# Performance work log

Hardware: AMD Instinct MI355X
Metric: run time of the kernel (lower is better)

## Reference

```python
import jax, jax.numpy as jnp
import numpy as np

B, T, N, D, FF, E, L, K = 4, 12, 2000, 16, 64, 4, 2, 2
EA, H = 3000, 3
BETA, CW = 0.01, 0.001


def setup_inputs() -> dict:
    key = jax.random.key(0)
    ks = iter(jax.random.split(key, 40))
    nrm = lambda shape, s=0.02: jax.random.normal(next(ks), shape, jnp.float32) * s
    inp = {}
    inp['x'] = jax.random.normal(next(ks), (B, T, N), jnp.float32)
    inp['velo'] = jax.random.uniform(next(ks), (B, T, N), jnp.float32)
    inp['adj_haversine'] = jax.random.uniform(next(ks), (N, N), jnp.float32) + 0.05
    inp['laplacian_diff'] = jax.random.normal(next(ks), (N, N), jnp.float32)
    inp['laplacian_heat'] = jax.random.normal(next(ks), (N, N), jnp.float32)
    inp['start_w'] = nrm((1, D)); inp['start_b'] = jnp.zeros((D,), jnp.float32)
    inp['gate_w'] = nrm((L, D, E))
    inp['exp_w1'] = nrm((L, E, D, FF)); inp['exp_b1'] = jnp.zeros((L, E, FF), jnp.float32)
    inp['exp_w2'] = nrm((L, E, FF, D)); inp['exp_b2'] = jnp.zeros((L, E, D), jnp.float32)
    inp['proj_w'] = nrm((T * D, T)); inp['proj_b'] = jnp.zeros((T,), jnp.float32)
    inp['lt_w'] = nrm((N, EA)); inp['lt_b'] = jnp.zeros((EA,), jnp.float32)
    inp['qkv_w'] = nrm((EA, 3 * EA)); inp['qkv_b'] = jnp.zeros((3 * EA,), jnp.float32)
    inp['attn_out_w'] = nrm((EA, EA)); inp['attn_out_b'] = jnp.zeros((EA,), jnp.float32)
    inp['ll_w'] = nrm((EA, N)); inp['ll_b'] = jnp.zeros((N,), jnp.float32)
    inp['p2_w'] = nrm((T, T)); inp['p2_b'] = jnp.zeros((T,), jnp.float32)
    return inp


def reference(x, velo, adj_haversine, laplacian_diff, laplacian_heat, start_w, start_b,
              gate_w, exp_w1, exp_b1, exp_w2, exp_b2, proj_w, proj_b, lt_w, lt_b,
              qkv_w, qkv_b, attn_out_w, attn_out_b, ll_w, ll_b, p2_w, p2_b):
    # start_fc: [B,T,N,1] -> [B,T,N,D]
    out = x[..., None] @ start_w + start_b
    balance = jnp.float32(0.0)
    cv = lambda v: v.var() / (v.mean() ** 2 + 1e-10)
    for l in range(L):  # AMS mixture-of-experts stack (noisy top-k gating, eval mode)
        feat = out.mean(axis=(1, 2))                      # [B,D]
        logits = feat @ gate_w[l]                          # [B,E]
        topv, topi = jax.lax.top_k(logits, K)
        g = jax.nn.softmax(topv, axis=-1)
        gates = jnp.zeros((B, E), out.dtype).at[jnp.arange(B)[:, None], topi].set(g)
        h = jax.nn.gelu(jnp.einsum('btnd,edf->ebtnf', out, exp_w1[l]) + exp_b1[l][:, None, None, None, :])
        y = jnp.einsum('ebtnf,efd->ebtnd', h, exp_w2[l]) + exp_b2[l][:, None, None, None, :]
        out = out + jnp.einsum('be,ebtnd->btnd', gates, y)  # residual_connection
        imp = gates.sum(0)
        load = (gates > 0).astype(out.dtype).sum(0)
        balance = balance + cv(imp) + cv(load)
    # wavelet layer: 1-level smoothing split along time
    low = lambda z: 0.5 * (z + jnp.roll(z, 1, axis=1))
    low_T = low(x)
    high_V = velo - low(velo)
    # navier-stokes-style graph laplacian from velocities
    v0 = velo[0, 0]                                        # [N]
    G = jnp.maximum(0.0, v0[:, None] / adj_haversine)
    G = jnp.where(jnp.isinf(G), 0.0, G)
    lap_ns = jnp.diag(G.sum(1)) - G
    std = lambda m: (m - m.mean()) / m.std()
    lap_d = std(laplacian_diff); lap_h = std(laplacian_heat)
    lap_ns = jnp.nan_to_num(std(lap_ns))
    # trunk projection: [B,T,N,D] -> [B,T,N]
    outp = (out.transpose(0, 2, 1, 3).reshape(B, N, T * D) @ proj_w + proj_b).transpose(0, 2, 1)
    # laplacian-fused matmuls
    r1 = low_T @ lap_d; r2 = high_V @ lap_ns; r3 = low_T @ lap_h
    rng01 = lambda m: (m - m.min()) / jnp.maximum(m.max() - m.min(), 1e-8)
    lin = lambda m: (rng01(m) @ lt_w + lt_b).transpose(1, 0, 2)   # [T,B,EA]
    r1, r2, r3 = lin(r1), lin(r2), lin(r3)
    hd = EA // H
    wq, wk, wv = jnp.split(qkv_w, 3, axis=1)
    bq, bk, bv = jnp.split(qkv_b, 3)
    def mha(q, k, v):
        qh = (q @ wq + bq).reshape(T, B, H, hd)
        kh = (k @ wk + bk).reshape(T, B, H, hd)
        vh = (v @ wv + bv).reshape(T, B, H, hd)
        sc = jnp.einsum('sbhd,tbhd->bhst', qh, kh) * (1.0 / np.sqrt(hd))
        a = jax.nn.softmax(sc, axis=-1)
        o = jnp.einsum('bhst,tbhd->sbhd', a, vh).reshape(T, B, EA)
        return o @ attn_out_w + attn_out_b
    o1 = mha(r1, r2, r3); o2 = mha(r2, r3, r1); o3 = mha(r3, r1, r2)
    back = lambda o: (o @ ll_w + ll_b).transpose(1, 0, 2)         # [B,T,N]
    out2 = BETA * (back(o1) + back(o2) + back(o3))
    out2 = (out2.reshape(-1, T) @ p2_w + p2_b).reshape(B, N, T).transpose(0, 2, 1)
    out_3 = outp + out2
    # contrastive loss between trunk and laplacian branch
    f1 = outp.transpose(0, 2, 1).reshape(B * N, T)
    f2 = out2.transpose(0, 2, 1).reshape(B * N, T)
    nz = lambda f: f / jnp.maximum(jnp.linalg.norm(f, axis=1, keepdims=True), 1e-12)
    sim = (nz(f1) @ nz(f2).T) / 0.1                               # [8000, 8000]
    closs = -jnp.mean(jnp.diagonal(jax.nn.log_softmax(sim, axis=1)))
    return out_3, balance, CW * closs
```

## Files before the change

### kernel.cpp

```cpp
#include <hip/hip_runtime.h>
#include <math.h>

namespace {
constexpr int B_ = 4, T_ = 12, N_ = 2000, D_ = 16, FF_ = 64, E_ = 4, L_ = 2;
constexpr int EA_ = 3000, H_ = 3, HD_ = EA_ / H_;
constexpr int BT_ = B_ * T_;
constexpr int R3_ = 3 * BT_;
constexpr long long NN_ = (long long)N_ * N_;
constexpr int BTN_ = B_ * T_ * N_;
constexpr float BETA_ = 0.01f, CW_ = 0.001f;
constexpr int RKS_ = 20;
constexpr int RKC_ = 100;
constexpr int KP3 = 3008;
constexpr int KP2 = 2016;

constexpr int W2_QN = 141, W2_QK = 47;
constexpr int W2_AN = 47,  W2_AK = 47;
constexpr int W2_LN = 32,  W2_LK = 47;
constexpr int W2_WN = 47,  W2_WK = 32;
constexpr int W2_C0 = W2_QN * W2_QK;
constexpr int W2_C1 = W2_C0 + W2_AN * W2_AK;
constexpr int W2_C2 = W2_C1 + W2_LN * W2_LK;
constexpr int W2_TOT = W2_C2 + W2_WN * W2_WK;

constexpr size_t OFF_OUT4 = 0;
constexpr size_t OFF_LOWT = OFF_OUT4 + (size_t)BTN_ * D_;
constexpr size_t OFF_HVT  = OFF_LOWT + BTN_;
constexpr size_t OFF_ALIN = OFF_HVT + BTN_;
constexpr size_t OFF_RT   = OFF_ALIN + (size_t)N_ * R3_;
constexpr size_t OFF_P    = OFF_RT + (size_t)EA_ * R3_;
constexpr size_t OFF_AOT  = OFF_P + (size_t)R3_ * 3 * EA_;
constexpr size_t OFF_OT   = OFF_AOT + (size_t)EA_ * R3_;
constexpr size_t OFF_O2P  = OFF_OT + (size_t)EA_ * R3_;
constexpr size_t OFF_OUTP = OFF_O2P + BTN_;
constexpr size_t OFF_O2F  = OFF_OUTP + BTN_;
constexpr size_t OFF_LI   = OFF_O2F + BTN_;
constexpr size_t OFF_S    = OFF_LI + 8000;
constexpr size_t OFF_RSL  = OFF_S + 2000;
constexpr size_t OFF_RSH  = OFF_RSL + 48;
constexpr size_t OFF_STP  = OFF_RSH + 48;
constexpr size_t OFF_STAT = OFF_STP + 3072;
constexpr size_t OFF_MMP  = OFF_STAT + 8;
constexpr size_t OFF_AB   = OFF_MMP + 384;
constexpr size_t OFF_CSP  = OFF_AB + 8;
constexpr size_t OFF_CS   = OFF_CSP + 48000;
constexpr size_t OFF_FEAT = OFF_CS + 3000;
constexpr size_t OFF_GATE = OFF_FEAT + 64;
constexpr size_t OFF_BAL  = OFF_GATE + 16;
constexpr size_t OFF_PART = ((OFF_BAL + 1 + 255) & ~(size_t)255);
constexpr size_t PARTCAP  = 6000000;
constexpr size_t OFF_BT_Q  = OFF_PART + PARTCAP;
constexpr size_t OFF_BT_A  = OFF_BT_Q + (size_t)9000 * KP3 / 2;
constexpr size_t OFF_BT_L  = OFF_BT_A + (size_t)3000 * KP3 / 2;
constexpr size_t OFF_BT_W  = OFF_BT_L + (size_t)2000 * KP3 / 2;
constexpr size_t OFF_AT_LIN= OFF_BT_W + (size_t)3000 * KP2 / 2;
constexpr size_t OFF_AT_Q  = OFF_AT_LIN + (size_t)R3_ * KP2 / 2;
constexpr size_t OFF_AT_AO = OFF_AT_Q + (size_t)R3_ * KP3 / 2;
constexpr size_t OFF_AT_LL = OFF_AT_AO + (size_t)R3_ * KP3 / 2;
constexpr size_t OFF_G1B   = OFF_AT_LL + (size_t)R3_ * KP3 / 2;
constexpr size_t OFF_G2B   = OFF_G1B + 128000;
}

typedef __attribute__((ext_vector_type(8))) short short8;
typedef __attribute__((ext_vector_type(4))) float f32x4;

__device__ __forceinline__ float waveReduceSum(float v) {
  for (int off = 32; off; off >>= 1) v += __shfl_down(v, off);
  return v;
}

__device__ __forceinline__ unsigned short f2bf(float x) {
  unsigned int u = __float_as_uint(x);
  unsigned int r = (u + 0x7FFFu + ((u >> 16) & 1u)) >> 16;
  return (unsigned short)r;
}

__device__ __forceinline__ void fma16(float* __restrict__ acc,
                                      const float4* __restrict__ a4, float bv) {
#pragma unroll
  for (int r4 = 0; r4 < 4; ++r4) {
    float4 av = a4[r4];
    acc[r4 * 4 + 0] = fmaf(av.x, bv, acc[r4 * 4 + 0]);
    acc[r4 * 4 + 1] = fmaf(av.y, bv, acc[r4 * 4 + 1]);
    acc[r4 * 4 + 2] = fmaf(av.z, bv, acc[r4 * 4 + 2]);
    acc[r4 * 4 + 3] = fmaf(av.w, bv, acc[r4 * 4 + 3]);
  }
}

__global__ void k_init(float* ws) {
  if (threadIdx.x == 0) ws[OFF_BAL] = 0.f;
}

__global__ void k_start(const float* __restrict__ x, const float* __restrict__ sw,
                        const float* __restrict__ sb, float* __restrict__ out4) {
  int i = blockIdx.x * 256 + threadIdx.x;
  if (i >= BTN_ * D_) return;
  int d = i & 15;
  out4[i] = fmaf(x[i >> 4], sw[d], sb[d]);
}

__global__ void k_feat(const float* __restrict__ out4, float* __restrict__ feat) {
  int b = blockIdx.x >> 4, d = blockIdx.x & 15;
  float s = 0.f;
  for (int tn = threadIdx.x; tn < T_ * N_; tn += 256)
    s += out4[((size_t)b * T_ * N_ + tn) * D_ + d];
  __shared__ float red[4];
  s = waveReduceSum(s);
  if ((threadIdx.x & 63) == 0) red[threadIdx.x >> 6] = s;
  __syncthreads();
  if (threadIdx.x == 0)
    feat[blockIdx.x] = (red[0] + red[1] + red[2] + red[3]) * (1.f / (T_ * N_));
}

__global__ void k_gate(const float* __restrict__ feat, const float* __restrict__ gw,
                       float* __restrict__ ws, int l) {
  __shared__ float lg[B_ * E_];
  int tid = threadIdx.x;
  if (tid < B_ * E_) {
    int b = tid >> 2, e = tid & 3;
    float s = 0.f;
    for (int d = 0; d < D_; ++d) s = fmaf(feat[b * D_ + d], gw[(l * D_ + d) * E_ + e], s);
    lg[tid] = s;
  }
  __syncthreads();
  if (tid == 0) {
    float* gates = ws + OFF_GATE;
    float imp[E_] = {0, 0, 0, 0}, load[E_] = {0, 0, 0, 0};
    for (int i = 0; i < B_ * E_; ++i) gates[i] = 0.f;
    for (int b = 0; b < B_; ++b) {
      const float* lb = lg + b * E_;
      int i1 = 0; float v1 = lb[0];
      for (int e = 1; e < E_; ++e) if (lb[e] > v1) { v1 = lb[e]; i1 = e; }
      int i2 = -1; float v2 = -1e30f;
      for (int e = 0; e < E_; ++e) { if (e == i1) continue; if (lb[e] > v2) { v2 = lb[e]; i2 = e; } }
      float e2 = expf(v2 - v1);
      float den = 1.f + e2;
      float g1 = 1.f / den, g2 = e2 / den;
      gates[b * E_ + i1] = g1; gates[b * E_ + i2] = g2;
      imp[i1] += g1; imp[i2] += g2; load[i1] += 1.f; load[i2] += 1.f;
    }
    float bal = 0.f;
    float m = 0.f; for (int e = 0; e < E_; ++e) m += imp[e]; m *= 0.25f;
    float v = 0.f; for (int e = 0; e < E_; ++e) { float d = imp[e] - m; v += d * d; } v *= 0.25f;
    bal += v / (m * m + 1e-10f);
    m = 0.f; for (int e = 0; e < E_; ++e) m += load[e]; m *= 0.25f;
    v = 0.f; for (int e = 0; e < E_; ++e) { float d = load[e] - m; v += d * d; } v *= 0.25f;
    bal += v / (m * m + 1e-10f);
    ws[OFF_BAL] += bal;
  }
}

__global__ void k_expert(float* __restrict__ out4, const float* __restrict__ w1,
                         const float* __restrict__ b1, const float* __restrict__ w2,
                         const float* __restrict__ b2, const float* __restrict__ ws, int l) {
  int b = blockIdx.y;
  int tn = blockIdx.x * 256 + threadIdx.x;
  if (tn >= T_ * N_) return;
  float* row = out4 + ((size_t)b * T_ * N_ + tn) * D_;
  float r[D_], acc[D_];
#pragma unroll
  for (int d = 0; d < D_; ++d) { r[d] = row[d]; acc[d] = r[d]; }
  const float* gates = ws + OFF_GATE;
  for (int e = 0; e < E_; ++e) {
    float g = gates[b * E_ + e];
    if (g <= 0.f) continue;
    const float* W1 = w1 + (size_t)(l * E_ + e) * D_ * FF_;
    const float* B1 = b1 + (size_t)(l * E_ + e) * FF_;
    const float* W2 = w2 + (size_t)(l * E_ + e) * FF_ * D_;
    const float* B2 = b2 + (size_t)(l * E_ + e) * D_;
#pragma unroll 4
    for (int f = 0; f < FF_; ++f) {
      float p = B1[f];
#pragma unroll
      for (int d = 0; d < D_; ++d) p = fmaf(r[d], W1[d * FF_ + f], p);
      float c2 = 1.5957691216057308f * (p + 0.044715f * p * p * p);
      float e1 = __expf(-c2);
      float hv = p * __builtin_amdgcn_rcpf(1.f + e1);
      float gh = g * hv;
#pragma unroll
      for (int d = 0; d < D_; ++d) acc[d] = fmaf(gh, W2[f * D_ + d], acc[d]);
    }
#pragma unroll
    for (int d = 0; d < D_; ++d) acc[d] = fmaf(g, B2[d], acc[d]);
  }
#pragma unroll
  for (int d = 0; d < D_; ++d) row[d] = acc[d];
}

__global__ void k_wavelet(const float* __restrict__ x, const float* __restrict__ velo,
                          float* __restrict__ lowT, float* __restrict__ hvT) {
  int i = blockIdx.x * 256 + threadIdx.x;
  if (i >= BTN_) return;
  int b = i / (T_ * N_);
  int t = (i / N_) % T_;
  int n = i % N_;
  int ip = b * T_ * N_ + ((t + T_ - 1) % T_) * N_ + n;
  int row = t * B_ + b;
  lowT[(size_t)n * BT_ + row] = 0.5f * (x[i] + x[ip]);
  hvT[(size_t)n * BT_ + row] = 0.5f * (velo[i] - velo[ip]);
}

__global__ void k_rowsum(const float* __restrict__ lowT, const float* __restrict__ hvT,
                         float* __restrict__ ws) {
  int which = blockIdx.x / BT_;
  int row = blockIdx.x % BT_;
  const float* M = which ? hvT : lowT;
  float s = 0.f;
  for (int n = threadIdx.x; n < N_; n += 256) s += M[(size_t)n * BT_ + row];
  __shared__ float red[4];
  s = waveReduceSum(s);
  if ((threadIdx.x & 63) == 0) red[threadIdx.x >> 6] = s;
  __syncthreads();
  if (threadIdx.x == 0) ws[(which ? OFF_RSH : OFF_RSL) + row] = red[0] + red[1] + red[2] + red[3];
}

__global__ void k_S(const float* __restrict__ adj, const float* __restrict__ v0,
                    float* __restrict__ S) {
  int m = blockIdx.x;
  float vm = v0[m];
  const float* a = adj + (size_t)m * N_;
  float s = 0.f;
  for (int n = threadIdx.x; n < N_; n += 256) s += vm / a[n];
  __shared__ float red[4];
  s = waveReduceSum(s);
  if ((threadIdx.x & 63) == 0) red[threadIdx.x >> 6] = s;
  __syncthreads();
  if (threadIdx.x == 0) S[m] = red[0] + red[1] + red[2] + red[3];
}

__global__ void k_stats3(const float* __restrict__ lapd, const float* __restrict__ laph,
                         const float* __restrict__ adj, const float* __restrict__ v0,
                         const float* __restrict__ S, float* __restrict__ stp) {
  int z = blockIdx.z;
  float s = 0.f, ss = 0.f;
  if (z < 2) {
    const float* M = z ? laph : lapd;
    for (long long i = blockIdx.x * 256 + threadIdx.x; i < NN_; i += 512 * 256) {
      float v = M[i];
      s += v; ss = fmaf(v, v, ss);
    }
  } else {
    for (long long i = blockIdx.x * 256 + threadIdx.x; i < NN_; i += 512 * 256) {
      int m = (int)(i / N_), n = (int)(i % N_);
      float e = -(v0[m] / adj[i]);
      if (m == n) e += S[m];
      s += e; ss = fmaf(e, e, ss);
    }
  }
  __shared__ float r1[4], r2[4];
  for (int off = 32; off; off >>= 1) { s += __shfl_down(s, off); ss += __shfl_down(ss, off); }
  if ((threadIdx.x & 63) == 0) { r1[threadIdx.x >> 6] = s; r2[threadIdx.x >> 6] = ss; }
  __syncthreads();
  if (threadIdx.x == 0) {
    float* p = stp + (size_t)z * 1024;
    p[blockIdx.x * 2] = r1[0] + r1[1] + r1[2] + r1[3];
    p[blockIdx.x * 2 + 1] = r2[0] + r2[1] + r2[2] + r2[3];
  }
}

__global__ void k_stats2(const float* __restrict__ stp, float* __restrict__ stat) {
  int z = blockIdx.x;
  const float* part = stp + (size_t)z * 1024;
  float s = 0.f, ss = 0.f;
  for (int i = threadIdx.x; i < 512; i += 256) { s += part[i * 2]; ss += part[i * 2 + 1]; }
  __shared__ float r1[4], r2[4];
  for (int off = 32; off; off >>= 1) { s += __shfl_down(s, off); ss += __shfl_down(ss, off); }
  if ((threadIdx.x & 63) == 0) { r1[threadIdx.x >> 6] = s; r2[threadIdx.x >> 6] = ss; }
  __syncthreads();
  if (threadIdx.x == 0) {
    float su = r1[0] + r1[1] + r1[2] + r1[3];
    float sq = r2[0] + r2[1] + r2[2] + r2[3];
    float mu = su * (1.f / (float)NN_);
    float var = sq * (1.f / (float)NN_) - mu * mu;
    stat[2 * z] = mu;
    stat[2 * z + 1] = 1.f / sqrtf(var);
  }
}

__global__ __launch_bounds__(256) void k_rgemm3(
    const float* __restrict__ lowT, const float* __restrict__ hvT,
    const float* __restrict__ lapd, const float* __restrict__ laph,
    const float* __restrict__ adj, const float* __restrict__ v0,
    const float* __restrict__ S, float* __restrict__ part) {
  int zz = blockIdx.z;
  int z = zz / 3, rg = zz % 3;
  int col = blockIdx.x * 256 + threadIdx.x;
  int m0 = blockIdx.y * RKC_;
  int m1 = min(N_, m0 + RKC_);
  float acc[16];
#pragma unroll
  for (int r = 0; r < 16; ++r) acc[r] = 0.f;
  if (col < N_) {
    const float* Abase = (z == 1 ? hvT : lowT);
    const float* ap = Abase + (size_t)m0 * BT_ + rg * 16;
    if (z != 1) {
      const float* Bm = z ? laph : lapd;
      const float* bp = Bm + (size_t)m0 * N_ + col;
      int len = m1 - m0;
      int ng = len >> 3;
      float bc[8];
      if (ng > 0) {
#pragma unroll
        for (int u = 0; u < 8; ++u) bc[u] = bp[(size_t)u * N_];
      }
      for (int gi = 0; gi < ng; ++gi) {
        float bn[8];
        bool more = (gi + 1 < ng);
        if (more) {
#pragma unroll
          for (int u = 0; u < 8; ++u) bn[u] = bp[(size_t)(8 + u) * N_];
        }
#pragma unroll
        for (int u = 0; u < 8; ++u)
          fma16(acc, (const float4*)(ap + (size_t)u * BT_), bc[u]);
        ap += (size_t)8 * BT_;
        bp += (size_t)8 * N_;
        if (more) {
#pragma unroll
          for (int u = 0; u < 8; ++u) bc[u] = bn[u];
        }
      }
      for (int m = m0 + (ng << 3); m < m1; ++m) {
        fma16(acc, (const float4*)ap, *bp);
        ap += BT_;
        bp += N_;
      }
    } else {
      const float* jp = adj + (size_t)m0 * N_ + col;
      int len = m1 - m0;
      int ng = len >> 3;
      float jc[8];
      if (ng > 0) {
#pragma unroll
        for (int u = 0; u < 8; ++u) jc[u] = jp[(size_t)u * N_];
      }
      int m = m0;
      for (int gi = 0; gi < ng; ++gi) {
        float jn[8];
        bool more = (gi + 1 < ng);
        if (more) {
#pragma unroll
          for (int u = 0; u < 8; ++u) jn[u] = jp[(size_t)(8 + u) * N_];
        }
#pragma unroll
        for (int u = 0; u < 8; ++u) {
          float bv = -(v0[m + u] / jc[u]);
          if (m + u == col) bv += S[m + u];
          fma16(acc, (const float4*)(ap + (size_t)u * BT_), bv);
        }
        m += 8;
        ap += (size_t)8 * BT_;
        jp += (size_t)8 * N_;
        if (more) {
#pragma unroll
          for (int u = 0; u < 8; ++u) jc[u] = jn[u];
        }
      }
      for (; m < m1; ++m) {
        float bv = -(v0[m] / (*jp));
        if (m == col) bv += S[m];
        fma16(acc, (const float4*)ap, bv);
        ap += BT_;
        jp += N_;
      }
    }
    float* pp = part + (((size_t)z * RKS_ + blockIdx.y) * BT_ + rg * 16) * N_ + col;
#pragma unroll
    for (int r = 0; r < 16; ++r) pp[(size_t)r * N_] = acc[r];
  }
}

__global__ void k_epiR3(const float* __restrict__ part, float* __restrict__ ws,
                        unsigned short* __restrict__ atl) {
  int z = blockIdx.z;
  int n = blockIdx.x * 256 + threadIdx.x;
  int row = blockIdx.y;
  if (n >= KP2) return;
  int arow = z * BT_ + row;
  if (n >= N_) { atl[(size_t)arow * KP2 + n] = 0; return; }
  const float* base = part + (size_t)z * RKS_ * BT_ * N_;
  float s = 0.f;
  for (int ks = 0; ks < RKS_; ++ks) s += base[((size_t)(ks * BT_ + row)) * N_ + n];
  int statIdx = (z == 0) ? 0 : (z == 1 ? 4 : 2);
  size_t rsOff = (z == 1) ? OFF_RSH : OFF_RSL;
  float mu = ws[OFF_STAT + statIdx], isd = ws[OFF_STAT + statIdx + 1];
  float val = (s - mu * ws[rsOff + row]) * isd;
  ws[OFF_ALIN + (size_t)n * R3_ + arow] = val;
  atl[(size_t)arow * KP2 + n] = f2bf(val);
}

__global__ __launch_bounds__(256) void k_wtrans4(
    const float* __restrict__ W0, const float* __restrict__ W1,
    const float* __restrict__ W2, const float* __restrict__ W3,
    unsigned short* __restrict__ T0, unsigned short* __restrict__ T1,
    unsigned short* __restrict__ T2, unsigned short* __restrict__ T3) {
  int bid = blockIdx.x;
  const float* W; unsigned short* Wt; int K, Nc, Kp, rel, NT;
  if (bid < W2_C0)      { W = W0; Wt = T0; K = EA_; Nc = 3 * EA_; Kp = KP3; rel = bid;         NT = W2_QN; }
  else if (bid < W2_C1) { W = W1; Wt = T1; K = EA_; Nc = EA_;     Kp = KP3; rel = bid - W2_C0; NT = W2_AN; }
  else if (bid < W2_C2) { W = W2; Wt = T2; K = EA_; Nc = N_;      Kp = KP3; rel = bid - W2_C1; NT = W2_LN; }
  else                  { W = W3; Wt = T3; K = N_;  Nc = EA_;     Kp = KP2; rel = bid - W2_C2; NT = W2_WN; }
  int kTile = rel / NT, nTile = rel % NT;
  int k0 = kTile * 64, n0 = nTile * 64;
  __shared__ float t[64][65];
  int nx = threadIdx.x & 15;
  int kk = threadIdx.x >> 4;
  bool fullN = (n0 + 64 <= Nc);
#pragma unroll
  for (int i = 0; i < 4; ++i) {
    int kl = kk + 16 * i;
    int k = k0 + kl;
    int n = n0 + 4 * nx;
    float4 v = {0.f, 0.f, 0.f, 0.f};
    if (k < K) {
      if (fullN) {
        v = *(const float4*)(W + (size_t)k * Nc + n);
      } else {
        if (n + 3 < Nc)      v = *(const float4*)(W + (size_t)k * Nc + n);
        else {
          if (n     < Nc) v.x = W[(size_t)k * Nc + n];
          if (n + 1 < Nc) v.y = W[(size_t)k * Nc + n + 1];
          if (n + 2 < Nc) v.z = W[(size_t)k * Nc + n + 2];
          if (n + 3 < Nc) v.w = W[(size_t)k * Nc + n + 3];
        }
      }
    }
    t[4 * nx + 0][kl] = v.x;
    t[4 * nx + 1][kl] = v.y;
    t[4 * nx + 2][kl] = v.z;
    t[4 * nx + 3][kl] = v.w;
  }
  __syncthreads();
  int kq = threadIdx.x & 15;
  int ny = threadIdx.x >> 4;
  int k = k0 + 4 * kq;
#pragma unroll
  for (int i = 0; i < 4; ++i) {
    int nl = ny + 16 * i;
    int n = n0 + nl;
    if (n < Nc && k + 3 < Kp) {
      unsigned int w0 = ((unsigned int)f2bf(t[nl][4 * kq + 1]) << 16) | f2bf(t[nl][4 * kq + 0]);
      unsigned int w1 = ((unsigned int)f2bf(t[nl][4 * kq + 3]) << 16) | f2bf(t[nl][4 * kq + 2]);
      uint2 u; u.x = w0; u.y = w1;
      *(uint2*)(Wt + (size_t)n * Kp + k) = u;
    }
  }
}

__global__ __launch_bounds__(256, 4) void k_mfma(
    const unsigned short* __restrict__ At, const unsigned short* __restrict__ Bt,
    float* __restrict__ part, int Nc, int Kp, int stepsTot, int stepChunk) {
  int lane = threadIdx.x & 63;
  int w = threadIdx.x >> 6;
  int lr = lane & 15, lo = lane >> 4;
  int gcol = blockIdx.x * 64 + w * 16 + lr;
  int bcol = min(gcol, Nc - 1);
  int s0 = blockIdx.y * stepChunk;
  int s1 = min(stepsTot, s0 + stepChunk);
  f32x4 acc[9];
#pragma unroll
  for (int mt = 0; mt < 9; ++mt) {
    acc[mt][0] = 0.f; acc[mt][1] = 0.f; acc[mt][2] = 0.f; acc[mt][3] = 0.f;
  }
  const unsigned short* bp = Bt + (size_t)bcol * Kp + (size_t)s0 * 32 + lo * 8;
  const unsigned short* ap = At + (size_t)lr * Kp + (size_t)s0 * 32 + lo * 8;
  for (int s = s0; s < s1; ++s) {
    short8 b = *(const short8*)bp;
#pragma unroll
    for (int mt = 0; mt < 9; ++mt) {
      short8 a = *(const short8*)(ap + (size_t)mt * 16 * Kp);
      acc[mt] = __builtin_amdgcn_mfma_f32_16x16x32_bf16(a, b, acc[mt], 0, 0, 0);
    }
    bp += 32;
    ap += 32;
  }
  if (gcol < Nc) {
#pragma unroll
    for (int mt = 0; mt < 9; ++mt) {
      int row = mt * 16 + lo * 4;
      float* pp = part + ((size_t)blockIdx.y * R3_ + row) * Nc + gcol;
      pp[0] = acc[mt][0];
      pp[(size_t)Nc] = acc[mt][1];
      pp[2 * (size_t)Nc] = acc[mt][2];
      pp[3 * (size_t)Nc] = acc[mt][3];
    }
  }
}

__global__ void k_minmax(const float* __restrict__ alin, float* __restrict__ mmp) {
  int g = blockIdx.y;
  float mn = 3.4e38f, mx = -3.4e38f;
  for (int i = blockIdx.x * 256 + threadIdx.x; i < N_ * BT_; i += 64 * 256) {
    int n = i / BT_, r = i % BT_;
    float v = alin[(size_t)n * R3_ + g * BT_ + r];
    mn = fminf(mn, v); mx = fmaxf(mx, v);
  }
  __shared__ float rn[4], rx[4];
  for (int off = 32; off; off >>= 1) {
    mn = fminf(mn, __shfl_down(mn, off));
    mx = fmaxf(mx, __shfl_down(mx, off));
  }
  if ((threadIdx.x & 63) == 0) { rn[threadIdx.x >> 6] = mn; rx[threadIdx.x >> 6] = mx; }
  __syncthreads();
  if (threadIdx.x == 0) {
    mn = fminf(fminf(rn[0], rn[1]), fminf(rn[2], rn[3]));
    mx = fmaxf(fmaxf(rx[0], rx[1]), fmaxf(rx[2], rx[3]));
    mmp[(size_t)(g * 64 + blockIdx.x) * 2] = mn;
    mmp[(size_t)(g * 64 + blockIdx.x) * 2 + 1] = mx;
  }
}

__global__ void k_minmax2(float* __restrict__ ws) {
  int g = blockIdx.x;
  int i = threadIdx.x;
  float mn = ws[OFF_MMP + (size_t)(g * 64 + i) * 2];
  float mx = ws[OFF_MMP + (size_t)(g * 64 + i) * 2 + 1];
  for (int off = 32; off; off >>= 1) {
    mn = fminf(mn, __shfl_down(mn, off));
    mx = fmaxf(mx, __shfl_down(mx, off));
  }
  if (i == 0) {
    float denom = fmaxf(mx - mn, 1e-8f);
    float a = 1.f / denom;
    ws[OFF_AB + g * 2] = a;
    ws[OFF_AB + g * 2 + 1] = -mn * a;
  }
}

__global__ void k_colsum(const float* __restrict__ ltw, float* __restrict__ csp) {
  int e = blockIdx.x * 256 + threadIdx.x;
  int ks = blockIdx.y;
  if (e >= EA_) return;
  float s = 0.f;
  for (int n = ks * 125; n < (ks + 1) * 125; ++n) s += ltw[(size_t)n * EA_ + e];
  csp[(size_t)ks * EA_ + e] = s;
}
__global__ void k_colsum2(float* __restrict__ ws) {
  int e = blockIdx.x * 256 + threadIdx.x;
  if (e >= EA_) return;
  float s = 0.f;
  for (int ks = 0; ks < 16; ++ks) s += ws[OFF_CSP + (size_t)ks * EA_ + e];
  ws[OFF_CS + e] = s;
}

__global__ void k_epiLin(const float* __restrict__ part, const float* __restrict__ ltb,
                         float* __restrict__ ws, unsigned short* __restrict__ atq,
                         int ksplit) {
  int e = blockIdx.x * 256 + threadIdx.x;
  int row = blockIdx.y;
  if (e >= KP3) return;
  if (e >= EA_) { atq[(size_t)row * KP3 + e] = 0; return; }
  float s = 0.f;
  for (int ks = 0; ks < ksplit; ++ks) s += part[((size_t)(ks * R3_ + row)) * EA_ + e];
  int g = row / BT_;
  float a = ws[OFF_AB + g * 2], bb = ws[OFF_AB + g * 2 + 1];
  float val = fmaf(a, s, fmaf(bb, ws[OFF_CS + e], ltb[e]));
  atq[(size_t)row * KP3 + e] = f2bf(val);
}

__global__ void k_epiQkv(const float* __restrict__ part, const float* __restrict__ qkvb,
                         float* __restrict__ P, int ksplit) {
  int c = blockIdx.x * 256 + threadIdx.x;
  int row = blockIdx.y;
  if (c >= 3 * EA_) return;
  float s = 0.f;
  for (int ks = 0; ks < ksplit; ++ks) s += part[((size_t)(ks * R3_ + row)) * (3 * EA_) + c];
  P[(size_t)row * (3 * EA_) + c] = s + qkvb[c];
}

__global__ void k_attn(const float* __restrict__ P, unsigned short* __restrict__ atao) {
  int mha = blockIdx.y;
  int s_ = blockIdx.x / (B_ * H_);
  int rem = blockIdx.x % (B_ * H_);
  int b = rem / H_, h = rem % H_;
  const int pq[3] = {0, 1, 2}, pk[3] = {1, 2, 0}, pv[3] = {2, 0, 1};
  const float* qrow = P + ((size_t)(pq[mha] * BT_ + s_ * B_ + b)) * (3 * EA_) + h * HD_;
  __shared__ float sc[T_];
  int w = threadIdx.x >> 6, lane = threadIdx.x & 63;
  for (int t = w; t < T_; t += 4) {
    const float* krow = P + ((size_t)(pk[mha] * BT_ + t * B_ + b)) * (3 * EA_) + EA_ + h * HD_;
    float p = 0.f;
    for (int d = lane; d < HD_; d += 64) p = fmaf(qrow[d], krow[d], p);
    p = waveReduceSum(p);
    if (lane == 0) sc[t] = p * 0.031622776601683794f;
  }
  __syncthreads();
  float a[T_];
  float m = sc[0];
#pragma unroll
  for (int t = 1; t < T_; ++t) m = fmaxf(m, sc[t]);
  float sum = 0.f;
#pragma unroll
  for (int t = 0; t < T_; ++t) { a[t] = expf(sc[t] - m); sum += a[t]; }
  float inv = 1.f / sum;
#pragma unroll
  for (int t = 0; t < T_; ++t) a[t] *= inv;
  int orow = mha * BT_ + s_ * B_ + b;
  for (int d = threadIdx.x; d < HD_; d += 256) {
    float o = 0.f;
#pragma unroll
    for (int t = 0; t < T_; ++t)
      o = fmaf(a[t], P[((size_t)(pv[mha] * BT_ + t * B_ + b)) * (3 * EA_) + 2 * EA_ + h * HD_ + d], o);
    atao[(size_t)orow * KP3 + h * HD_ + d] = f2bf(o);
  }
  if (h == 0 && threadIdx.x < 8) atao[(size_t)orow * KP3 + EA_ + threadIdx.x] = 0;
}

__global__ void k_epiAO(const float* __restrict__ part, const float* __restrict__ aob,
                        unsigned short* __restrict__ atll, int ksplit) {
  int c = blockIdx.x * 256 + threadIdx.x;
  int row = blockIdx.y;
  if (c >= KP3) return;
  if (c >= EA_) { atll[(size_t)row * KP3 + c] = 0; return; }
  float s = 0.f;
  for (int ks = 0; ks < ksplit; ++ks) s += part[((size_t)(ks * R3_ + row)) * EA_ + c];
  atll[(size_t)row * KP3 + c] = f2bf(s + aob[c]);
}

__global__ void k_epiLL(const float* __restrict__ part, const float* __restrict__ llb,
                        float* __restrict__ o2p, int ksplit) {
  int n = blockIdx.x * 256 + threadIdx.x;
  int row = blockIdx.y;
  if (n >= N_) return;
  float s = 0.f;
  for (int g = 0; g < 3; ++g)
    for (int ks = 0; ks < ksplit; ++ks)
      s += part[((size_t)(ks * R3_ + g * BT_ + row)) * N_ + n];
  int t = row / B_, b = row % B_;
  o2p[(size_t)b * (T_ * N_) + t * N_ + n] = BETA_ * (s + 3.f * llb[n]);
}

__global__ void k_proj(const float* __restrict__ out4, const float* __restrict__ pw,
                       const float* __restrict__ pb, float* __restrict__ outp) {
  int i = blockIdx.x * 256 + threadIdx.x;
  if (i >= BTN_) return;
  int b = i / (T_ * N_);
  int t = (i / N_) % T_;
  int n = i % N_;
  float acc = pb[t];
  for (int t2 = 0; t2 < T_; ++t2) {
    const float* o = out4 + ((size_t)(b * T_ + t2) * N_ + n) * D_;
#pragma unroll
    for (int d = 0; d < D_; ++d) acc = fmaf(o[d], pw[(t2 * D_ + d) * T_ + t], acc);
  }
  outp[i] = acc;
}

__global__ void k_p2(const float* __restrict__ o2p, const float* __restrict__ p2w,
                     const float* __restrict__ p2b, float* __restrict__ o2f) {
  int i = blockIdx.x * 256 + threadIdx.x;
  if (i >= BTN_) return;
  int b = i / (T_ * N_);
  int t = (i / N_) % T_;
  int n = i % N_;
  float acc = p2b[t];
  const float* src = o2p + (size_t)b * (T_ * N_) + (size_t)n * T_;
#pragma unroll
  for (int c = 0; c < T_; ++c) acc = fmaf(src[c], p2w[c * T_ + t], acc);
  o2f[i] = acc;
}

__global__ void k_fng(const float* __restrict__ outp, const float* __restrict__ o2f,
                      float* __restrict__ dout, unsigned short* __restrict__ g1b,
                      unsigned short* __restrict__ g2b) {
  int r = blockIdx.x * 256 + threadIdx.x;
  if (r >= B_ * N_) return;
  int b = r / N_, n = r % N_;
  float v1[T_], v2[T_];
  float s1 = 0.f, s2 = 0.f;
#pragma unroll
  for (int t = 0; t < T_; ++t) {
    size_t idx = (size_t)b * T_ * N_ + (size_t)t * N_ + n;
    v1[t] = outp[idx];
    v2[t] = o2f[idx];
    dout[idx] = v1[t] + v2[t];
    s1 = fmaf(v1[t], v1[t], s1);
    s2 = fmaf(v2[t], v2[t], s2);
  }
  float n1 = fmaxf(sqrtf(s1), 1e-12f), n2 = fmaxf(sqrtf(s2), 1e-12f);
  float i1 = 10.f / n1, i2 = 1.f / n2;
  unsigned short q[32], z[32];
#pragma unroll
  for (int t = 0; t < T_; ++t) { q[t] = f2bf(v1[t] * i1); z[t] = f2bf(v2[t] * i2); }
#pragma unroll
  for (int t = T_; t < 32; ++t) { q[t] = 0; z[t] = 0; }
  short8* qd = (short8*)(g1b + (size_t)r * 32);
  short8* zd = (short8*)(g2b + (size_t)r * 32);
#pragma unroll
  for (int c = 0; c < 4; ++c) {
    short8 pv, pz;
#pragma unroll
    for (int e = 0; e < 8; ++e) { pv[e] = (short)q[c * 8 + e]; pz[e] = (short)z[c * 8 + e]; }
    qd[c] = pv;
    zd[c] = pz;
  }
}

__global__ __launch_bounds__(256) void k_lsemf(const unsigned short* __restrict__ g1b,
                                               const unsigned short* __restrict__ g2b,
                                               float* __restrict__ psm,
                                               float* __restrict__ psd) {
  int lane = threadIdx.x & 63, w = threadIdx.x >> 6;
  int lr = lane & 15, lo = lane >> 4;
  int i0 = blockIdx.x * 16;
  int slice = blockIdx.y * 4 + w;
  short8 a = *(const short8*)(g1b + (size_t)(i0 + lr) * 32 + lo * 8);
  float sm[4] = {0.f, 0.f, 0.f, 0.f};
  float sd[4] = {0.f, 0.f, 0.f, 0.f};
  for (int t = slice; t < 500; t += 16) {
    int j0 = t * 16;
    short8 b = *(const short8*)(g2b + (size_t)(j0 + lr) * 32 + lo * 8);
    f32x4 acc = {0.f, 0.f, 0.f, 0.f};
    acc = __builtin_amdgcn_mfma_f32_16x16x32_bf16(a, b, acc, 0, 0, 0);
#pragma unroll
    for (int rg = 0; rg < 4; ++rg) {
      float s = acc[rg];
      sm[rg] += __expf(s);
      if (j0 + lr == i0 + lo * 4 + rg) sd[rg] = s;
    }
  }
#pragma unroll
  for (int off = 1; off < 16; off <<= 1) {
#pragma unroll
    for (int rg = 0; rg < 4; ++rg) {
      sm[rg] += __shfl_xor(sm[rg], off);
      sd[rg] += __shfl_xor(sd[rg], off);
    }
  }
  __shared__ float lsm[4][16], lsd[4][16];
  if (lr == 0) {
#pragma unroll
    for (int rg = 0; rg < 4; ++rg) {
      lsm[w][lo * 4 + rg] = sm[rg];
      lsd[w][lo * 4 + rg] = sd[rg];
    }
  }
  __syncthreads();
  if (threadIdx.x < 16) {
    float m = lsm[0][threadIdx.x] + lsm[1][threadIdx.x] + lsm[2][threadIdx.x] + lsm[3][threadIdx.x];
    float d = lsd[0][threadIdx.x] + lsd[1][threadIdx.x] + lsd[2][threadIdx.x] + lsd[3][threadIdx.x];
    psm[(size_t)blockIdx.y * 8000 + i0 + threadIdx.x] = m;
    psd[(size_t)blockIdx.y * 8000 + i0 + threadIdx.x] = d;
  }
}

__global__ __launch_bounds__(1024) void k_lsefin(const float* __restrict__ psm,
                                                 const float* __restrict__ psd,
                                                 const float* __restrict__ ws,
                                                 float* __restrict__ dout) {
  float acc = 0.f;
  for (int r = threadIdx.x; r < B_ * N_; r += 1024) {
    float sm = psm[r] + psm[8000 + r] + psm[16000 + r] + psm[24000 + r];
    float sd = psd[r] + psd[8000 + r] + psd[16000 + r] + psd[24000 + r];
    acc += sd - logf(sm);
  }
  __shared__ float red[16];
  acc = waveReduceSum(acc);
  if ((threadIdx.x & 63) == 0) red[threadIdx.x >> 6] = acc;
  __syncthreads();
  if (threadIdx.x == 0) {
    float s = 0.f;
    for (int i = 0; i < 16; ++i) s += red[i];
    float closs = -s * (1.f / (B_ * N_));
    dout[BTN_] = ws[OFF_BAL];
    dout[BTN_ + 1] = CW_ * closs;
  }
}

extern "C" void kernel_launch(void* const* d_in, const int* in_sizes, int n_in,
                              void* d_out, int out_size, void* d_ws, size_t ws_size,
                              hipStream_t stream) {
  const float* x    = (const float*)d_in[0];
  const float* velo = (const float*)d_in[1];
  const float* adj  = (const float*)d_in[2];
  const float* lapd = (const float*)d_in[3];
  const float* laph = (const float*)d_in[4];
  const float* sw   = (const float*)d_in[5];
  const float* sb   = (const float*)d_in[6];
  const float* gw   = (const float*)d_in[7];
  const float* ew1  = (const float*)d_in[8];
  const float* eb1  = (const float*)d_in[9];
  const float* ew2  = (const float*)d_in[10];
  const float* eb2  = (const float*)d_in[11];
  const float* pw   = (const float*)d_in[12];
  const float* pb   = (const float*)d_in[13];
  const float* ltw  = (const float*)d_in[14];
  const float* ltb  = (const float*)d_in[15];
  const float* qkvw = (const float*)d_in[16];
  const float* qkvb = (const float*)d_in[17];
  const float* aow  = (const float*)d_in[18];
  const float* aob  = (const float*)d_in[19];
  const float* llw  = (const float*)d_in[20];
  const float* llb  = (const float*)d_in[21];
  const float* p2w  = (const float*)d_in[22];
  const float* p2b  = (const float*)d_in[23];
  float* ws = (float*)d_ws;
  float* dout = (float*)d_out;
  const float* v0 = velo;
  float* part = ws + OFF_PART;
  unsigned short* btQ  = (unsigned short*)(ws + OFF_BT_Q);
  unsigned short* btA  = (unsigned short*)(ws + OFF_BT_A);
  unsigned short* btL  = (unsigned short*)(ws + OFF_BT_L);
  unsigned short* btW  = (unsigned short*)(ws + OFF_BT_W);
  unsigned short* atLin = (unsigned short*)(ws + OFF_AT_LIN);
  unsigned short* atQ   = (unsigned short*)(ws + OFF_AT_Q);
  unsigned short* atAO  = (unsigned short*)(ws + OFF_AT_AO);
  unsigned short* atLL  = (unsigned short*)(ws + OFF_AT_LL);
  unsigned short* g1b   = (unsigned short*)(ws + OFF_G1B);
  unsigned short* g2b   = (unsigned short*)(ws + OFF_G2B);
  dim3 b256(256);

  k_init<<<dim3(1), dim3(64), 0, stream>>>(ws);

  k_wtrans4<<<dim3(W2_TOT), b256, 0, stream>>>(qkvw, aow, llw, ltw, btQ, btA, btL, btW);

  k_start<<<dim3((BTN_ * D_ + 255) / 256), b256, 0, stream>>>(x, sw, sb, ws + OFF_OUT4);

  for (int l = 0; l < L_; ++l) {
    k_feat<<<dim3(B_ * D_), b256, 0, stream>>>(ws + OFF_OUT4, ws + OFF_FEAT);
    k_gate<<<dim3(1), dim3(64), 0, stream>>>(ws + OFF_FEAT, gw, ws, l);
    k_expert<<<dim3((T_ * N_ + 255) / 256, B_), b256, 0, stream>>>(ws + OFF_OUT4, ew1, eb1, ew2, eb2, ws, l);
  }

  k_wavelet<<<dim3((BTN_ + 255) / 256), b256, 0, stream>>>(x, velo, ws + OFF_LOWT, ws + OFF_HVT);
  k_rowsum<<<dim3(2 * BT_), b256, 0, stream>>>(ws + OFF_LOWT, ws + OFF_HVT, ws);
  k_S<<<dim3(N_), b256, 0, stream>>>(adj, v0, ws + OFF_S);

  k_stats3<<<dim3(512, 1, 3), b256, 0, stream>>>(lapd, laph, adj, v0, ws + OFF_S, ws + OFF_STP);
  k_stats2<<<dim3(3), b256, 0, stream>>>(ws + OFF_STP, ws + OFF_STAT);

  k_rgemm3<<<dim3(8, RKS_, 9), b256, 0, stream>>>(ws + OFF_LOWT, ws + OFF_HVT, lapd, laph,
                                                  adj, v0, ws + OFF_S, part);
  k_epiR3<<<dim3(8, 48, 3), b256, 0, stream>>>(part, ws, atLin);

  k_minmax<<<dim3(64, 3), b256, 0, stream>>>(ws + OFF_ALIN, ws + OFF_MMP);
  k_minmax2<<<dim3(3), dim3(64), 0, stream>>>(ws);
  k_colsum<<<dim3(12, 16), b256, 0, stream>>>(ltw, ws + OFF_CSP);
  k_colsum2<<<dim3(12), b256, 0, stream>>>(ws);

  k_mfma<<<dim3(47, 12), b256, 0, stream>>>(atLin, btW, part, EA_, KP2, KP2 / 32, 6);
  k_epiLin<<<dim3(12, 144), b256, 0, stream>>>(part, ltb, ws, atQ, 12);

  k_mfma<<<dim3(141, 4), b256, 0, stream>>>(atQ, btQ, part, 3 * EA_, KP3, KP3 / 32, 24);
  k_epiQkv<<<dim3(36, 144), b256, 0, stream>>>(part, qkvb, ws + OFF_P, 4);

  k_attn<<<dim3(T_ * B_ * H_, 3), b256, 0, stream>>>(ws + OFF_P, atAO);

  k_mfma<<<dim3(47, 12), b256, 0, stream>>>(atAO, btA, part, EA_, KP3, KP3 / 32, 8);
  k_epiAO<<<dim3(12, 144), b256, 0, stream>>>(part, aob, atLL, 12);

  k_mfma<<<dim3(32, 16), b256, 0, stream>>>(atLL, btL, part, N_, KP3, KP3 / 32, 6);
  k_epiLL<<<dim3(8, 48), b256, 0, stream>>>(part, llb, ws + OFF_O2P, 16);

  k_proj<<<dim3((BTN_ + 255) / 256), b256, 0, stream>>>(ws + OFF_OUT4, pw, pb, ws + OFF_OUTP);
  k_p2<<<dim3((BTN_ + 255) / 256), b256, 0, stream>>>(ws + OFF_O2P, p2w, p2b, ws + OFF_O2F);

  k_fng<<<dim3((B_ * N_ + 255) / 256), b256, 0, stream>>>(ws + OFF_OUTP, ws + OFF_O2F, dout, g1b, g2b);

  k_lsemf<<<dim3(500, 4), b256, 0, stream>>>(g1b, g2b, part, part + 32000);
  k_lsefin<<<dim3(1), dim3(1024), 0, stream>>>(part, part + 32000, ws, dout);
}
```

Before: 586.8 us.

## Fuse fp32-to-bf16 weight transpose into MFMA GEMM via LDS staging

Removes the separate weight transpose/convert kernel and instead has the GEMM kernel load fp32 weights directly, convert them to bf16 and stage them transposed in double-buffered LDS per K-step. This removes writing and re-reading a full bf16 copy of all large weight matrices each call. In exchange, each K-step now needs a block-wide barrier and conversion work inside the GEMM loop.

Result: faster. 555.5 us (-5.3%).

```diff
diff --git a/kernel.cpp b/kernel.cpp
--- a/kernel.cpp
+++ b/kernel.cpp
@@ -13,15 +13,6 @@
 constexpr int RKC_ = 100;
 constexpr int KP3 = 3008;
 constexpr int KP2 = 2016;
-
-constexpr int W2_QN = 141, W2_QK = 47;
-constexpr int W2_AN = 47,  W2_AK = 47;
-constexpr int W2_LN = 32,  W2_LK = 47;
-constexpr int W2_WN = 47,  W2_WK = 32;
-constexpr int W2_C0 = W2_QN * W2_QK;
-constexpr int W2_C1 = W2_C0 + W2_AN * W2_AK;
-constexpr int W2_C2 = W2_C1 + W2_LN * W2_LK;
-constexpr int W2_TOT = W2_C2 + W2_WN * W2_WK;
 
 constexpr size_t OFF_OUT4 = 0;
 constexpr size_t OFF_LOWT = OFF_OUT4 + (size_t)BTN_ * D_;
@@ -49,11 +40,7 @@
 constexpr size_t OFF_BAL  = OFF_GATE + 16;
 constexpr size_t OFF_PART = ((OFF_BAL + 1 + 255) & ~(size_t)255);
 constexpr size_t PARTCAP  = 6000000;
-constexpr size_t OFF_BT_Q  = OFF_PART + PARTCAP;
-constexpr size_t OFF_BT_A  = OFF_BT_Q + (size_t)9000 * KP3 / 2;
-constexpr size_t OFF_BT_L  = OFF_BT_A + (size_t)3000 * KP3 / 2;
-constexpr size_t OFF_BT_W  = OFF_BT_L + (size_t)2000 * KP3 / 2;
-constexpr size_t OFF_AT_LIN= OFF_BT_W + (size_t)3000 * KP2 / 2;
+constexpr size_t OFF_AT_LIN= OFF_PART + PARTCAP;
 constexpr size_t OFF_AT_Q  = OFF_AT_LIN + (size_t)R3_ * KP2 / 2;
 constexpr size_t OFF_AT_AO = OFF_AT_Q + (size_t)R3_ * KP3 / 2;
 constexpr size_t OFF_AT_LL = OFF_AT_AO + (size_t)R3_ * KP3 / 2;
@@ -389,91 +376,75 @@
   atl[(size_t)arow * KP2 + n] = f2bf(val);
 }
 
-__global__ __launch_bounds__(256) void k_wtrans4(
-    const float* __restrict__ W0, const float* __restrict__ W1,
-    const float* __restrict__ W2, const float* __restrict__ W3,
-    unsigned short* __restrict__ T0, unsigned short* __restrict__ T1,
-    unsigned short* __restrict__ T2, unsigned short* __restrict__ T3) {
-  int bid = blockIdx.x;
-  const float* W; unsigned short* Wt; int K, Nc, Kp, rel, NT;
-  if (bid < W2_C0)      { W = W0; Wt = T0; K = EA_; Nc = 3 * EA_; Kp = KP3; rel = bid;         NT = W2_QN; }
-  else if (bid < W2_C1) { W = W1; Wt = T1; K = EA_; Nc = EA_;     Kp = KP3; rel = bid - W2_C0; NT = W2_AN; }
-  else if (bid < W2_C2) { W = W2; Wt = T2; K = EA_; Nc = N_;      Kp = KP3; rel = bid - W2_C1; NT = W2_LN; }
-  else                  { W = W3; Wt = T3; K = N_;  Nc = EA_;     Kp = KP2; rel = bid - W2_C2; NT = W2_WN; }
-  int kTile = rel / NT, nTile = rel % NT;
-  int k0 = kTile * 64, n0 = nTile * 64;
-  __shared__ float t[64][65];
-  int nx = threadIdx.x & 15;
-  int kk = threadIdx.x >> 4;
-  bool fullN = (n0 + 64 <= Nc);
-#pragma unroll
-  for (int i = 0; i < 4; ++i) {
-    int kl = kk + 16 * i;
-    int k = k0 + kl;
-    int n = n0 + 4 * nx;
-    float4 v = {0.f, 0.f, 0.f, 0.f};
-    if (k < K) {
-      if (fullN) {
-        v = *(const float4*)(W + (size_t)k * Nc + n);
-      } else {
-        if (n + 3 < Nc)      v = *(const float4*)(W + (size_t)k * Nc + n);
-        else {
-          if (n     < Nc) v.x = W[(size_t)k * Nc + n];
-          if (n + 1 < Nc) v.y = W[(size_t)k * Nc + n + 1];
-          if (n + 2 < Nc) v.z = W[(size_t)k * Nc + n + 2];
-          if (n + 3 < Nc) v.w = W[(size_t)k * Nc + n + 3];
+__global__ __launch_bounds__(256) void k_mfmaW(
+    const unsigned short* __restrict__ At, const float* __restrict__ W,
+    float* __restrict__ part, int Nc, int Kp, int K, int stepChunk) {
+  __shared__ unsigned int lds[2][64][21];
+  int tid = threadIdx.x;
+  int lane = tid & 63, w = tid >> 6;
+  int lr = lane & 15, lo = lane >> 4;
+  int colBase = blockIdx.x * 64;
+  int gcol = colBase + w * 16 + lr;
+  int stepsTot = Kp / 32;
+  int s0 = blockIdx.y * stepChunk;
+  int s1 = min(stepsTot, s0 + stepChunk);
+  int cg = tid & 15, kr2 = tid >> 4;
+  int c0l = 4 * cg;
+  bool fullC = (colBase + 64 <= Nc);
+
+  f32x4 acc[9];
+#pragma unroll
+  for (int mt = 0; mt < 9; ++mt) {
+    acc[mt][0] = 0.f; acc[mt][1] = 0.f; acc[mt][2] = 0.f; acc[mt][3] = 0.f;
+  }
+
+  auto stage = [&](int s, int buf) {
+    int kA = s * 32 + 2 * kr2;
+    int kB = kA + 1;
+    float4 r0 = {0.f, 0.f, 0.f, 0.f}, r1 = {0.f, 0.f, 0.f, 0.f};
+    int c0 = colBase + c0l;
+    if (fullC) {
+      if (kA < K) r0 = *(const float4*)(W + (size_t)kA * Nc + c0);
+      if (kB < K) r1 = *(const float4*)(W + (size_t)kB * Nc + c0);
+    } else {
+      float rr0[4] = {0.f, 0.f, 0.f, 0.f}, rr1[4] = {0.f, 0.f, 0.f, 0.f};
+#pragma unroll
+      for (int e = 0; e < 4; ++e) {
+        if (c0 + e < Nc) {
+          if (kA < K) rr0[e] = W[(size_t)kA * Nc + c0 + e];
+          if (kB < K) rr1[e] = W[(size_t)kB * Nc + c0 + e];
         }
       }
-    }
-    t[4 * nx + 0][kl] = v.x;
-    t[4 * nx + 1][kl] = v.y;
-    t[4 * nx + 2][kl] = v.z;
-    t[4 * nx + 3][kl] = v.w;
-  }
-  __syncthreads();
-  int kq = threadIdx.x & 15;
-  int ny = threadIdx.x >> 4;
-  int k = k0 + 4 * kq;
-#pragma unroll
-  for (int i = 0; i < 4; ++i) {
-    int nl = ny + 16 * i;
-    int n = n0 + nl;
-    if (n < Nc && k + 3 < Kp) {
-      unsigned int w0 = ((unsigned int)f2bf(t[nl][4 * kq + 1]) << 16) | f2bf(t[nl][4 * kq + 0]);
-      unsigned int w1 = ((unsigned int)f2bf(t[nl][4 * kq + 3]) << 16) | f2bf(t[nl][4 * kq + 2]);
-      uint2 u; u.x = w0; u.y = w1;
-      *(uint2*)(Wt + (size_t)n * Kp + k) = u;
-    }
-  }
-}
-
-__global__ __launch_bounds__(256, 4) void k_mfma(
-    const unsigned short* __restrict__ At, const unsigned short* __restrict__ Bt,
-    float* __restrict__ part, int Nc, int Kp, int stepsTot, int stepChunk) {
-  int lane = threadIdx.x & 63;
-  int w = threadIdx.x >> 6;
-  int lr = lane & 15, lo = lane >> 4;
-  int gcol = blockIdx.x * 64 + w * 16 + lr;
-  int bcol = min(gcol, Nc - 1);
-  int s0 = blockIdx.y * stepChunk;
-  int s1 = min(stepsTot, s0 + stepChunk);
-  f32x4 acc[9];
-#pragma unroll
-  for (int mt = 0; mt < 9; ++mt) {
-    acc[mt][0] = 0.f; acc[mt][1] = 0.f; acc[mt][2] = 0.f; acc[mt][3] = 0.f;
-  }
-  const unsigned short* bp = Bt + (size_t)bcol * Kp + (size_t)s0 * 32 + lo * 8;
+      r0.x = rr0[0]; r0.y = rr0[1]; r0.z = rr0[2]; r0.w = rr0[3];
+      r1.x = rr1[0]; r1.y = rr1[1]; r1.z = rr1[2]; r1.w = rr1[3];
+    }
+    lds[buf][c0l + 0][kr2] = ((unsigned int)f2bf(r1.x) << 16) | f2bf(r0.x);
+    lds[buf][c0l + 1][kr2] = ((unsigned int)f2bf(r1.y) << 16) | f2bf(r0.y);
+    lds[buf][c0l + 2][kr2] = ((unsigned int)f2bf(r1.z) << 16) | f2bf(r0.z);
+    lds[buf][c0l + 3][kr2] = ((unsigned int)f2bf(r1.w) << 16) | f2bf(r0.w);
+  };
+
+  if (s0 < s1) stage(s0, 0);
+  __syncthreads();
+
   const unsigned short* ap = At + (size_t)lr * Kp + (size_t)s0 * 32 + lo * 8;
+  int lcol = w * 16 + lr;
   for (int s = s0; s < s1; ++s) {
-    short8 b = *(const short8*)bp;
+    int buf = (s - s0) & 1;
+    union { unsigned int u[4]; short8 s8; } bu;
+#pragma unroll
+    for (int j = 0; j < 4; ++j) bu.u[j] = lds[buf][lcol][lo * 4 + j];
+    short8 b = bu.s8;
 #pragma unroll
     for (int mt = 0; mt < 9; ++mt) {
       short8 a = *(const short8*)(ap + (size_t)mt * 16 * Kp);
       acc[mt] = __builtin_amdgcn_mfma_f32_16x16x32_bf16(a, b, acc[mt], 0, 0, 0);
     }
-    bp += 32;
+    if (s + 1 < s1) stage(s + 1, buf ^ 1);
+    __syncthreads();
     ap += 32;
   }
+
   if (gcol < Nc) {
 #pragma unroll
     for (int mt = 0; mt < 9; ++mt) {
@@ -798,10 +769,6 @@
   float* dout = (float*)d_out;
   const float* v0 = velo;
   float* part = ws + OFF_PART;
-  unsigned short* btQ  = (unsigned short*)(ws + OFF_BT_Q);
-  unsigned short* btA  = (unsigned short*)(ws + OFF_BT_A);
-  unsigned short* btL  = (unsigned short*)(ws + OFF_BT_L);
-  unsigned short* btW  = (unsigned short*)(ws + OFF_BT_W);
   unsigned short* atLin = (unsigned short*)(ws + OFF_AT_LIN);
   unsigned short* atQ   = (unsigned short*)(ws + OFF_AT_Q);
   unsigned short* atAO  = (unsigned short*)(ws + OFF_AT_AO);
@@ -812,8 +779,6 @@
 
   k_init<<<dim3(1), dim3(64), 0, stream>>>(ws);
 
-  k_wtrans4<<<dim3(W2_TOT), b256, 0, stream>>>(qkvw, aow, llw, ltw, btQ, btA, btL, btW);
-
   k_start<<<dim3((BTN_ * D_ + 255) / 256), b256, 0, stream>>>(x, sw, sb, ws + OFF_OUT4);
 
   for (int l = 0; l < L_; ++l) {
@@ -838,18 +803,18 @@
   k_colsum<<<dim3(12, 16), b256, 0, stream>>>(ltw, ws + OFF_CSP);
   k_colsum2<<<dim3(12), b256, 0, stream>>>(ws);
 
-  k_mfma<<<dim3(47, 12), b256, 0, stream>>>(atLin, btW, part, EA_, KP2, KP2 / 32, 6);
+  k_mfmaW<<<dim3(47, 12), b256, 0, stream>>>(atLin, ltw, part, EA_, KP2, N_, 6);
   k_epiLin<<<dim3(12, 144), b256, 0, stream>>>(part, ltb, ws, atQ, 12);
 
-  k_mfma<<<dim3(141, 4), b256, 0, stream>>>(atQ, btQ, part, 3 * EA_, KP3, KP3 / 32, 24);
+  k_mfmaW<<<dim3(141, 4), b256, 0, stream>>>(atQ, qkvw, part, 3 * EA_, KP3, EA_, 24);
   k_epiQkv<<<dim3(36, 144), b256, 0, stream>>>(part, qkvb, ws + OFF_P, 4);
 
   k_attn<<<dim3(T_ * B_ * H_, 3), b256, 0, stream>>>(ws + OFF_P, atAO);
 
-  k_mfma<<<dim3(47, 12), b256, 0, stream>>>(atAO, btA, part, EA_, KP3, KP3 / 32, 8);
+  k_mfmaW<<<dim3(47, 12), b256, 0, stream>>>(atAO, aow, part, EA_, KP3, EA_, 8);
   k_epiAO<<<dim3(12, 144), b256, 0, stream>>>(part, aob, atLL, 12);
 
-  k_mfma<<<dim3(32, 16), b256, 0, stream>>>(atLL, btL, part, N_, KP3, KP3 / 32, 6);
+  k_mfmaW<<<dim3(32, 16), b256, 0, stream>>>(atLL, llw, part, N_, KP3, EA_, 6);
   k_epiLL<<<dim3(8, 48), b256, 0, stream>>>(part, llb, ws + OFF_O2P, 16);
 
   k_proj<<<dim3((BTN_ + 255) / 256), b256, 0, stream>>>(ws + OFF_OUT4, pw, pb, ws + OFF_OUTP);
```
